# Kernel optimization log

Measured on AMD Instinct MI355X. Metric: run time of the kernel, lower is better.

## Reference

```python
import jax, jax.numpy as jnp
import numpy as np

EMBED_DIM = 256
NUM_HEADS = 8
HEAD_DIM = 32
BIAS_HIDDEN = 64
LN_EPS = 1e-5


def setup_inputs() -> dict:
    key = jax.random.key(0)
    ks = jax.random.split(key, 12)
    B, N = 2, 1024
    inner = NUM_HEADS * HEAD_DIM  # 256
    inp = {
        'x': jax.random.normal(ks[0], (B, N, EMBED_DIM), dtype=jnp.float32),
        'coords': jax.random.normal(ks[1], (B, N, 2), dtype=jnp.float32),
        'velocities': jax.random.normal(ks[2], (B, N, 2), dtype=jnp.float32),
        # LayerNorm params
        'ln_g': jnp.ones((EMBED_DIM,), jnp.float32),
        'ln_b': jnp.zeros((EMBED_DIM,), jnp.float32),
        # qkv projection (no bias)
        'w_qkv': jax.random.normal(ks[3], (EMBED_DIM, 3 * inner), dtype=jnp.float32) * (EMBED_DIM ** -0.5),
        # output projection
        'w_o': jax.random.normal(ks[4], (inner, EMBED_DIM), dtype=jnp.float32) * (inner ** -0.5),
        'b_o': jnp.zeros((EMBED_DIM,), jnp.float32),
        # relational bias MLP: Linear(5,64) -> GELU -> Linear(64, num_heads)
        'w1': jax.random.normal(ks[5], (5, BIAS_HIDDEN), dtype=jnp.float32) * (5 ** -0.5),
        'b1': jnp.zeros((BIAS_HIDDEN,), jnp.float32),
        'w2': jax.random.normal(ks[6], (BIAS_HIDDEN, NUM_HEADS), dtype=jnp.float32) * (BIAS_HIDDEN ** -0.5),
        'b2': jnp.zeros((NUM_HEADS,), jnp.float32),
    }
    return inp


def _rope_sin_cos(n, dim):
    half = dim // 2  # rotary applied over half pairs
    inv_freq = 1.0 / (10000.0 ** (jnp.arange(0, half, dtype=jnp.float32) / half))
    freqs = jnp.arange(n, dtype=jnp.float32)[:, None] * inv_freq[None, :]  # [n, half]
    return jnp.sin(freqs), jnp.cos(freqs)


def _apply_rope(t, sin, cos):
    d = t.shape[-1]
    t1, t2 = t[..., : d // 2], t[..., d // 2 :]
    return jnp.concatenate([t1 * cos - t2 * sin, t2 * cos + t1 * sin], axis=-1)


def reference(x, coords, velocities, ln_g, ln_b, w_qkv, w_o, b_o, w1, b1, w2, b2):
    b, n, _ = x.shape
    # LayerNorm
    mu = jnp.mean(x, axis=-1, keepdims=True)
    var = jnp.mean((x - mu) ** 2, axis=-1, keepdims=True)
    h = (x - mu) / jnp.sqrt(var + LN_EPS) * ln_g + ln_b
    # qkv
    qkv = h @ w_qkv  # [b, n, 3*inner]
    inner = NUM_HEADS * HEAD_DIM
    q, k, v = jnp.split(qkv, 3, axis=-1)
    reshape_heads = lambda t: t.reshape(b, n, NUM_HEADS, HEAD_DIM).transpose(0, 2, 1, 3)
    q, k, v = reshape_heads(q), reshape_heads(k), reshape_heads(v)  # [b,h,n,d]
    sin, cos = _rope_sin_cos(n, HEAD_DIM)  # [n, d//2], broadcast over b,h
    q = _apply_rope(q, sin, cos)
    k = _apply_rope(k, sin, cos)
    scale = HEAD_DIM ** -0.5
    scores = jnp.einsum('bhnd,bhmd->bhnm', q, k) * scale  # [b,h,n,n] fp32
    # relational bias: pairwise MLP over [dx(2), |dx|(1), dv(2)]
    dx = coords[:, :, None, :] - coords[:, None, :, :]        # [b,n,n,2]
    dist = jnp.linalg.norm(dx, axis=-1, keepdims=True)        # [b,n,n,1]
    dv = velocities[:, :, None, :] - velocities[:, None, :, :]
    feats = jnp.concatenate([dx, dist, dv], axis=-1)          # [b,n,n,5]
    hid = jax.nn.gelu(feats @ w1 + b1, approximate=False)     # [b,n,n,64]
    rel = (hid @ w2 + b2).transpose(0, 3, 1, 2)               # [b,h,n,n]
    scores = scores + rel
    probs = jax.nn.softmax(scores, axis=-1)
    probs = jnp.nan_to_num(probs, nan=0.0)
    out = jnp.einsum('bhnm,bhmd->bhnd', probs, v)
    out = out.transpose(0, 2, 1, 3).reshape(b, n, inner)
    return out @ w_o + b_o
```

## Files before the change

kernel.cpp:

```cpp
#include <hip/hip_runtime.h>
#include <hip/hip_bf16.h>
#include <hip/hip_fp16.h>
#include <math.h>
#include <string.h>

typedef _Float16 half8 __attribute__((ext_vector_type(8)));
typedef _Float16 half4 __attribute__((ext_vector_type(4)));
typedef float floatx4 __attribute__((ext_vector_type(4)));
typedef float floatx16 __attribute__((ext_vector_type(16)));

#if defined(__has_builtin) && __has_builtin(__builtin_amdgcn_mfma_f32_16x16x16f16)
#define MFMA_PV(a, b, c) __builtin_amdgcn_mfma_f32_16x16x16f16((a), (b), (c), 0, 0, 0)
#else
__device__ __forceinline__ floatx4 mfma_pv_asm(half4 a, half4 b, floatx4 c) {
  floatx4 d;
  asm volatile("v_mfma_f32_16x16x16_f16 %0, %1, %2, %3"
               : "=v"(d) : "v"(a), "v"(b), "v"(c));
  return d;
}
#define MFMA_PV(a, b, c) mfma_pv_asm((a), (b), (c))
#endif

__device__ __forceinline__ floatx16 MFMA_S1(half4 a, half4 b, floatx16 c) {
#if defined(__has_builtin) && __has_builtin(__builtin_amdgcn_mfma_f32_32x32x8f16)
  return __builtin_amdgcn_mfma_f32_32x32x8f16(a, b, c, 0, 0, 0);
#else
  floatx16 d;
  asm volatile("v_mfma_f32_32x32x8_f16 %0, %1, %2, %3"
               : "=v"(d) : "v"(a), "v"(b), "v"(c));
  return d;
#endif
}

__device__ __forceinline__ floatx16 MFMA_S2(half8 a, half8 b, floatx16 c) {
#if defined(__has_builtin) && __has_builtin(__builtin_amdgcn_mfma_f32_32x32x16_f16)
  return __builtin_amdgcn_mfma_f32_32x32x16_f16(a, b, c, 0, 0, 0);
#else
  floatx16 d;
  asm volatile("v_mfma_f32_32x32x16_f16 %0, %1, %2, %3"
               : "=v"(d) : "v"(a), "v"(b), "v"(c));
  return d;
#endif
}

__device__ __forceinline__ float gelu_exact(float z) {
  return 0.5f * z * (1.0f + erff(z * 0.70710678118654752f));
}
__device__ __forceinline__ unsigned int packh2(float a, float b) {
  __half2 h = __halves2half2(__float2half_rn(a), __float2half_rn(b));
  unsigned int u;
  memcpy(&u, &h, 4);
  return u;
}

__global__ __launch_bounds__(256) void prep_kernel(
    const float* __restrict__ x, const float* __restrict__ g,
    const float* __restrict__ bv, __half* __restrict__ h16,
    const float* __restrict__ w_qkv, const float* __restrict__ w_o,
    const float* __restrict__ w1, const float* __restrict__ b1,
    const float* __restrict__ w2,
    __half* __restrict__ wqT, __half* __restrict__ woT,
    unsigned int* __restrict__ gtabu, uint2* __restrict__ A1g,
    uint4* __restrict__ A2g) {
  int t = threadIdx.x;
  if (blockIdx.x < 2048) {
    int row = blockIdx.x;
    float v = x[(size_t)row * 256 + t];
    float s = v, q = v * v;
#pragma unroll
    for (int o = 32; o > 0; o >>= 1) {
      s += __shfl_xor(s, o);
      q += __shfl_xor(q, o);
    }
    __shared__ float ss[4], qq[4];
    int w = t >> 6, l = t & 63;
    if (l == 0) { ss[w] = s; qq[w] = q; }
    __syncthreads();
    s = ss[0] + ss[1] + ss[2] + ss[3];
    q = qq[0] + qq[1] + qq[2] + qq[3];
    float mu = s * (1.f / 256.f);
    float var = q * (1.f / 256.f) - mu * mu;
    float inv = rsqrtf(var + 1e-5f);
    h16[(size_t)row * 256 + t] = __float2half_rn((v - mu) * inv * g[t] + bv[t]);
    return;
  }
  int bx = blockIdx.x - 2048;
  if (bx < 768) {
    wqT[(size_t)bx * 256 + t] = __float2half_rn(w_qkv[(size_t)t * 768 + bx]);
  } else if (bx < 1024) {
    int n = bx - 768;
    woT[(size_t)n * 256 + t] = __float2half_rn(w_o[(size_t)t * 256 + n]);
  } else if (bx == 1024) {
#pragma unroll
    for (int s = 0; s < 8; s++) {
      int e = t * 8 + s;
      float z = -16.f + (float)e * (1.f / 64.f);
      float g0 = gelu_exact(z);
      float g1 = gelu_exact(z + (1.f / 64.f));
      gtabu[e] = packh2(g0, g1 - g0);
    }
  } else {
    if (t < 128) {
      int hb = t >> 6, l = t & 63;
      int hid = hb * 32 + (l & 31);
      float v[4];
#pragma unroll
      for (int e = 0; e < 4; e++) {
        int k = (l >> 5) * 4 + e;
        v[e] = (k < 5) ? w1[k * 64 + hid] : ((k == 5) ? b1[hid] : 0.f);
      }
      A1g[t] = make_uint2(packh2(v[0], v[1]), packh2(v[2], v[3]));
    }
    {
      int c = t >> 6, l = t & 63;
      int row = l & 31;
      int lh = l >> 5;
      float v[8];
#pragma unroll
      for (int e = 0; e < 8; e++) {
        int hid = c * 16 + (e & 3) + 8 * (e >> 2) + 4 * lh;
        v[e] = (row < 8) ? w2[hid * 8 + row] : 0.f;
      }
      A2g[t] = make_uint4(packh2(v[0], v[1]), packh2(v[2], v[3]),
                          packh2(v[4], v[5]), packh2(v[6], v[7]));
    }
  }
}

__global__ __launch_bounds__(256) void qkv_rope(
    const __half* __restrict__ h16, const __half* __restrict__ wqT,
    __half* __restrict__ qo, __half* __restrict__ ko, __half* __restrict__ vo) {
  int wave = blockIdx.x * 4 + (threadIdx.x >> 6);
  int mt = wave / 24, nt = wave - mt * 24;
  int l = threadIdx.x & 63;
  int c31 = l & 31, kg = l >> 5;
  int m0 = mt * 32, n0 = nt * 32;
  floatx16 acc0 = {0.f}, acc1 = {0.f};
  const _Float16* ap = (const _Float16*)h16 + (size_t)(m0 + c31) * 256 + kg * 8;
  const _Float16* bp = (const _Float16*)wqT + (size_t)(n0 + c31) * 256 + kg * 8;
  for (int k0 = 0; k0 < 256; k0 += 32) {
    half8 a0 = *(const half8*)(ap + k0);
    half8 b0 = *(const half8*)(bp + k0);
    half8 a1 = *(const half8*)(ap + k0 + 16);
    half8 b1 = *(const half8*)(bp + k0 + 16);
    acc0 = MFMA_S2(a0, b0, acc0);
    acc1 = MFMA_S2(a1, b1, acc1);
  }
  floatx16 acc = acc0 + acc1;

  if (nt < 16) {
    __half* dst = (nt < 8) ? qo : ko;
    float qscale = (nt < 8) ? 0.17677669529663687f : 1.0f;
    int hh = nt & 7;
    int f = c31 & 15;
    float inv_freq = exp2f((float)f * -0.8304820237218407f);
#pragma unroll
    for (int r = 0; r < 16; r++) {
      float part = __shfl_xor(acc[r], 16);
      int m = m0 + (r & 3) + 8 * (r >> 2) + 4 * kg;
      int nseq = m & 1023, bb = m >> 10;
      float sn, cs;
      __sincosf((float)nseq * inv_freq, &sn, &cs);
      float out = (c31 < 16) ? (acc[r] * cs - part * sn)
                             : (acc[r] * cs + part * sn);
      dst[((size_t)(bb * 8 + hh) * 1024 + nseq) * 32 + c31] =
          __float2half_rn(out * qscale);
    }
  } else {
    int hh = nt - 16;
#pragma unroll
    for (int r = 0; r < 16; r++) {
      int m = m0 + (r & 3) + 8 * (r >> 2) + 4 * kg;
      int nseq = m & 1023, bb = m >> 10;
      vo[((size_t)(bb * 8 + hh) * 1024 + nseq) * 32 + c31] = __float2half_rn(acc[r]);
    }
  }
}

__device__ __forceinline__ _Float16 gelu_tab16(float z, const unsigned int* gt) {
  float tf = __builtin_amdgcn_fmed3f(fmaf(z, 64.f, 1024.f), 0.f, 2047.f);
  float fr = __builtin_amdgcn_fractf(tf);
  unsigned int e = gt[(unsigned int)tf];
  union { unsigned int u; _Float16 h[2]; } cv;
  cv.u = e;
  return (_Float16)(cv.h[0] + (_Float16)fr * cv.h[1]);
}

__global__ __launch_bounds__(512) void fused_attn(
    const __half* __restrict__ qh, const __half* __restrict__ kh,
    const __half* __restrict__ vh,
    const float* __restrict__ coords, const float* __restrict__ vels,
    const unsigned int* __restrict__ gtabu, const uint2* __restrict__ A1g,
    const uint4* __restrict__ A2g, const float* __restrict__ b2,
    float* __restrict__ Opart, float* __restrict__ ml) {
  __shared__ unsigned int gtab[2048];
  __shared__ __half relS[8][64][18];
  const int t = threadIdx.x;
  for (int e = t; e < 2048; e += 512) gtab[e] = gtabu[e];

  const int js = blockIdx.x & 7;
  const int it = (blockIdx.x >> 3) & 63;
  const int b  = blockIdx.x >> 9;
  const int h  = t >> 6;
  const int lane = t & 63;
  const int lg = lane >> 4, li16 = lane & 15;
  const int li = lane & 31, lh = lane >> 5;
  const int i0 = it * 16;
  const size_t bh = (size_t)(b * 8 + h) * 1024;

  float b2v0 = b2[4 * lh + 0], b2v1 = b2[4 * lh + 1];
  float b2v2 = b2[4 * lh + 2], b2v3 = b2[4 * lh + 3];

  const half8 qf = *(const half8*)((const _Float16*)qh + (bh + i0 + li16) * 32 + 8 * lg);
  floatx4 accLo = {0.f, 0.f, 0.f, 0.f};
  floatx4 accHi = {0.f, 0.f, 0.f, 0.f};
  float m_run = -3.0e38f, l_run = 0.f;

  __syncthreads();

  for (int chunk = 0; chunk < 2; chunk++) {
    const int jt = js * 128 + chunk * 64;
    {
      uint2 a1u0 = A1g[lane], a1u1 = A1g[64 + lane];
      uint4 a2u0 = A2g[lane], a2u1 = A2g[64 + lane];
      uint4 a2u2 = A2g[128 + lane], a2u3 = A2g[192 + lane];
#pragma unroll
      for (int tt = 0; tt < 4; tt++) {
        const int i_loc = 2 * h + (tt >> 1);
        const int jsub = tt & 1;
        const int i = i0 + i_loc;
        const int j = jt + jsub * 32 + li;
        float2 ci = *(const float2*)&coords[(size_t)(b * 1024 + i) * 2];
        float2 vi = *(const float2*)&vels[(size_t)(b * 1024 + i) * 2];
        float2 cj = *(const float2*)&coords[(size_t)(b * 1024 + j) * 2];
        float2 vj = *(const float2*)&vels[(size_t)(b * 1024 + j) * 2];
        float dx0 = ci.x - cj.x, dx1 = ci.y - cj.y;
        float dv0 = vi.x - vj.x, dv1 = vi.y - vj.y;
        float dist = sqrtf(dx0 * dx0 + dx1 * dx1);
        half4 bf;
        bf[0] = lh ? (_Float16)dv1 : (_Float16)dx0;
        bf[1] = lh ? (_Float16)1.0f : (_Float16)dx1;
        bf[2] = lh ? (_Float16)0.0f : (_Float16)dist;
        bf[3] = lh ? (_Float16)0.0f : (_Float16)dv0;

        floatx16 zinit = {0.f};
        floatx16 acc = {0.f};
        {
          floatx16 z0 = MFMA_S1(*(half4*)&a1u0, bf, zinit);
          unsigned int u[8] __attribute__((aligned(16)));
#pragma unroll
          for (int q = 0; q < 8; q++) {
            _Float16 ga = gelu_tab16(z0[2 * q], gtab);
            _Float16 gb = gelu_tab16(z0[2 * q + 1], gtab);
            union { unsigned int uu; _Float16 hx[2]; } cv;
            cv.hx[0] = ga; cv.hx[1] = gb;
            u[q] = cv.uu;
          }
          acc = MFMA_S2(*(half8*)&a2u0, *(half8*)&u[0], acc);
          acc = MFMA_S2(*(half8*)&a2u1, *(half8*)&u[4], acc);
        }
        {
          floatx16 z1 = MFMA_S1(*(half4*)&a1u1, bf, zinit);
          unsigned int u[8] __attribute__((aligned(16)));
#pragma unroll
          for (int q = 0; q < 8; q++) {
            _Float16 ga = gelu_tab16(z1[2 * q], gtab);
            _Float16 gb = gelu_tab16(z1[2 * q + 1], gtab);
            union { unsigned int uu; _Float16 hx[2]; } cv;
            cv.hx[0] = ga; cv.hx[1] = gb;
            u[q] = cv.uu;
          }
          acc = MFMA_S2(*(half8*)&a2u2, *(half8*)&u[0], acc);
          acc = MFMA_S2(*(half8*)&a2u3, *(half8*)&u[4], acc);
        }
        const int jc = jsub * 32 + li;
        relS[4 * lh + 0][jc][i_loc] = __float2half_rn(acc[0] + b2v0);
        relS[4 * lh + 1][jc][i_loc] = __float2half_rn(acc[1] + b2v1);
        relS[4 * lh + 2][jc][i_loc] = __float2half_rn(acc[2] + b2v2);
        relS[4 * lh + 3][jc][i_loc] = __float2half_rn(acc[3] + b2v3);
      }
    }
    __syncthreads();
    {
      const _Float16* kb = (const _Float16*)kh + (bh + jt + li16) * 32 + 8 * lg;
      half8 kf0 = *(const half8*)(kb + 0 * 512);
      half8 kf1 = *(const half8*)(kb + 1 * 512);
      half8 kf2 = *(const half8*)(kb + 2 * 512);
      half8 kf3 = *(const half8*)(kb + 3 * 512);
      floatx4 c0, c1, c2, c3;
#pragma unroll
      for (int r = 0; r < 4; r++) {
        c0[r] = __half2float(relS[h][0 + 4 * lg + r][li16]);
        c1[r] = __half2float(relS[h][16 + 4 * lg + r][li16]);
        c2[r] = __half2float(relS[h][32 + 4 * lg + r][li16]);
        c3[r] = __half2float(relS[h][48 + 4 * lg + r][li16]);
      }
      __builtin_amdgcn_s_setprio(1);
      floatx4 st0 = __builtin_amdgcn_mfma_f32_16x16x32_f16(kf0, qf, c0, 0, 0, 0);
      floatx4 st1 = __builtin_amdgcn_mfma_f32_16x16x32_f16(kf1, qf, c1, 0, 0, 0);
      floatx4 st2 = __builtin_amdgcn_mfma_f32_16x16x32_f16(kf2, qf, c2, 0, 0, 0);
      floatx4 st3 = __builtin_amdgcn_mfma_f32_16x16x32_f16(kf3, qf, c3, 0, 0, 0);
      __builtin_amdgcn_s_setprio(0);
      float s[16];
#pragma unroll
      for (int r = 0; r < 4; r++) {
        s[0 + r] = st0[r]; s[4 + r] = st1[r];
        s[8 + r] = st2[r]; s[12 + r] = st3[r];
      }
      float tm = fmaxf(fmaxf(fmaxf(s[0], s[1]), fmaxf(s[2], s[3])),
                       fmaxf(fmaxf(s[4], s[5]), fmaxf(s[6], s[7])));
      tm = fmaxf(tm, fmaxf(fmaxf(fmaxf(s[8], s[9]), fmaxf(s[10], s[11])),
                           fmaxf(fmaxf(s[12], s[13]), fmaxf(s[14], s[15]))));
      tm = fmaxf(tm, __shfl_xor(tm, 16));
      tm = fmaxf(tm, __shfl_xor(tm, 32));
      float nm = fmaxf(m_run, tm);
      float fc = __expf(m_run - nm);
      float p[16];
#pragma unroll
      for (int e = 0; e < 16; e++) p[e] = __expf(s[e] - nm);
      float ts = ((p[0] + p[1]) + (p[2] + p[3])) + ((p[4] + p[5]) + (p[6] + p[7]));
      ts += ((p[8] + p[9]) + (p[10] + p[11])) + ((p[12] + p[13]) + (p[14] + p[15]));
      ts += __shfl_xor(ts, 16);
      ts += __shfl_xor(ts, 32);
      l_run = l_run * fc + ts;
      m_run = nm;
      float fT0 = __shfl(fc, 4 * lg + 0);
      float fT1 = __shfl(fc, 4 * lg + 1);
      float fT2 = __shfl(fc, 4 * lg + 2);
      float fT3 = __shfl(fc, 4 * lg + 3);
      accLo[0] *= fT0; accHi[0] *= fT0;
      accLo[1] *= fT1; accHi[1] *= fT1;
      accLo[2] *= fT2; accHi[2] *= fT2;
      accLo[3] *= fT3; accHi[3] *= fT3;
#pragma unroll
      for (int tt = 0; tt < 4; tt++) {
        half4 pf;
        pf[0] = (_Float16)p[4 * tt + 0];
        pf[1] = (_Float16)p[4 * tt + 1];
        pf[2] = (_Float16)p[4 * tt + 2];
        pf[3] = (_Float16)p[4 * tt + 3];
        const _Float16* vb = (const _Float16*)vh + (bh + jt + tt * 16 + 4 * lg) * 32 + li16;
        half4 vf0, vf1;
        vf0[0] = vb[0];  vf0[1] = vb[32]; vf0[2] = vb[64]; vf0[3] = vb[96];
        vf1[0] = vb[16]; vf1[1] = vb[48]; vf1[2] = vb[80]; vf1[3] = vb[112];
        __builtin_amdgcn_s_setprio(1);
        accLo = MFMA_PV(pf, vf0, accLo);
        accHi = MFMA_PV(pf, vf1, accHi);
        __builtin_amdgcn_s_setprio(0);
      }
    }
    __syncthreads();
  }
  size_t orow = (size_t)(b * 8 + js) * 1024 + i0 + 4 * lg;
#pragma unroll
  for (int r = 0; r < 4; r++) {
    float* op = Opart + (orow + r) * 256 + h * 32 + li16;
    op[0] = accLo[r];
    op[16] = accHi[r];
  }
  if (lane < 16) {
    ((float2*)ml)[((size_t)(b * 8 + js) * 1024 + i0 + lane) * 8 + h] =
        make_float2(m_run, l_run);
  }
}

__global__ __launch_bounds__(256) void combine_proj(
    const float* __restrict__ Opart, const float* __restrict__ ml,
    const __half* __restrict__ woT, const float* __restrict__ b_o,
    float* __restrict__ out) {
  __shared__ _Float16 As[16][264];
  const int r0 = blockIdx.x * 8;
  const int t = threadIdx.x;
  const int hh = t >> 5;
#pragma unroll
  for (int rr = 8; rr < 16; rr++) As[rr][t] = (_Float16)0.f;
#pragma unroll
  for (int rr = 0; rr < 8; rr++) {
    int row = r0 + rr;
    int b = row >> 10, i = row & 1023;
    float2 mls[8];
    float M = -1e30f;
#pragma unroll
    for (int js = 0; js < 8; js++) {
      mls[js] = ((const float2*)ml)[(((size_t)(b * 8 + js) * 1024) + i) * 8 + hh];
      M = fmaxf(M, mls[js].x);
    }
    float L = 0.f, Ov = 0.f;
#pragma unroll
    for (int js = 0; js < 8; js++) {
      float w = __expf(mls[js].x - M);
      L += mls[js].y * w;
      Ov += Opart[(((size_t)(b * 8 + js) * 1024) + i) * 256 + t] * w;
    }
    As[rr][t] = (_Float16)(Ov / L);
  }
  __syncthreads();
  const int wv = t >> 6, lane = t & 63;
  const int lg = lane >> 4, li = lane & 15;
#pragma unroll
  for (int nt = 0; nt < 4; nt++) {
    int n0 = (wv * 4 + nt) * 16;
    floatx4 acc = {0.f, 0.f, 0.f, 0.f};
    const _Float16* bp = (const _Float16*)woT + (size_t)(n0 + li) * 256 + 8 * lg;
#pragma unroll
    for (int k0 = 0; k0 < 256; k0 += 32) {
      half8 af = *(const half8*)&As[li][k0 + 8 * lg];
      half8 bf = *(const half8*)(bp + k0);
      acc = __builtin_amdgcn_mfma_f32_16x16x32_f16(af, bf, acc, 0, 0, 0);
    }
    float bb = b_o[n0 + li];
#pragma unroll
    for (int r = 0; r < 4; r++) {
      int mrow = 4 * lg + r;
      if (mrow < 8) out[(size_t)(r0 + mrow) * 256 + n0 + li] = acc[r] + bb;
    }
  }
}

extern "C" void kernel_launch(void* const* d_in, const int* in_sizes, int n_in,
                              void* d_out, int out_size, void* d_ws, size_t ws_size,
                              hipStream_t stream) {
  const float* x      = (const float*)d_in[0];
  const float* coords = (const float*)d_in[1];
  const float* vels   = (const float*)d_in[2];
  const float* ln_g   = (const float*)d_in[3];
  const float* ln_b   = (const float*)d_in[4];
  const float* w_qkv  = (const float*)d_in[5];
  const float* w_o    = (const float*)d_in[6];
  const float* b_o    = (const float*)d_in[7];
  const float* w1     = (const float*)d_in[8];
  const float* b1     = (const float*)d_in[9];
  const float* w2     = (const float*)d_in[10];
  const float* b2     = (const float*)d_in[11];
  float* out = (float*)d_out;

  char* wsb = (char*)d_ws;
  float* Opart = (float*)wsb;
  __half* wqT  = (__half*)(wsb + 16777216);
  __half* woT  = (__half*)(wsb + 17170432);
  unsigned int* gtab = (unsigned int*)(wsb + 17301504);
  uint2* A1g   = (uint2*)(wsb + 17317888);
  uint4* A2g   = (uint4*)(wsb + 17318912);
  __half* h16  = (__half*)(wsb + 17825792);
  __half* qh   = (__half*)(wsb + 18874368);
  __half* kh   = (__half*)(wsb + 19922944);
  __half* vh   = (__half*)(wsb + 20971520);
  float* ml    = (float*)(wsb + 22020096);

  prep_kernel<<<3074, 256, 0, stream>>>(x, ln_g, ln_b, h16, w_qkv, w_o,
                                        w1, b1, w2, wqT, woT, gtab, A1g, A2g);
  qkv_rope<<<384, 256, 0, stream>>>(h16, wqT, qh, kh, vh);
  fused_attn<<<1024, 512, 0, stream>>>(qh, kh, vh, coords, vels, gtab,
                                       A1g, A2g, b2, Opart, ml);
  combine_proj<<<256, 256, 0, stream>>>(Opart, ml, woT, b_o, out);
}
```

Before: 79.99 us.

## Double-buffer relational bias tile and overlap MLP with attention phase

Doubles the shared bias buffer so the bias MLP for the second key chunk is computed while the first chunk's QK/softmax/PV phase runs. This removes one of the block barriers and lets MFMA and gather work from the two phases interleave. The bias-MLP weight fragments are also loaded once before the chunks instead of once per chunk. In exchange, shared memory use and register pressure go up, which may lower occupancy.

```diff
diff --git a/kernel.cpp b/kernel.cpp
--- a/kernel.cpp
+++ b/kernel.cpp
@@ -194,7 +194,7 @@
     const uint4* __restrict__ A2g, const float* __restrict__ b2,
     float* __restrict__ Opart, float* __restrict__ ml) {
   __shared__ unsigned int gtab[2048];
-  __shared__ __half relS[8][64][18];
+  __shared__ __half relS[2][8][64][18];
   const int t = threadIdx.x;
   for (int e = t; e < 2048; e += 512) gtab[e] = gtabu[e];
 
@@ -216,141 +216,150 @@
   floatx4 accHi = {0.f, 0.f, 0.f, 0.f};
   float m_run = -3.0e38f, l_run = 0.f;
 
+  uint2 a1u0 = A1g[lane], a1u1 = A1g[64 + lane];
+  uint4 a2u0 = A2g[lane], a2u1 = A2g[64 + lane];
+  uint4 a2u2 = A2g[128 + lane], a2u3 = A2g[192 + lane];
+
+#define PHASE_A(CHUNK, BUF)                                                    \
+  {                                                                            \
+    const int jtA = js * 128 + (CHUNK) * 64;                                   \
+    _Pragma("unroll")                                                          \
+    for (int tt = 0; tt < 4; tt++) {                                           \
+      const int i_loc = 2 * h + (tt >> 1);                                     \
+      const int jsub = tt & 1;                                                 \
+      const int iA = i0 + i_loc;                                               \
+      const int jA = jtA + jsub * 32 + li;                                     \
+      float2 ci = *(const float2*)&coords[(size_t)(b * 1024 + iA) * 2];        \
+      float2 vi = *(const float2*)&vels[(size_t)(b * 1024 + iA) * 2];          \
+      float2 cj = *(const float2*)&coords[(size_t)(b * 1024 + jA) * 2];        \
+      float2 vj = *(const float2*)&vels[(size_t)(b * 1024 + jA) * 2];          \
+      float dx0 = ci.x - cj.x, dx1 = ci.y - cj.y;                              \
+      float dv0 = vi.x - vj.x, dv1 = vi.y - vj.y;                              \
+      float dist = sqrtf(dx0 * dx0 + dx1 * dx1);                               \
+      half4 bf;                                                                \
+      bf[0] = lh ? (_Float16)dv1 : (_Float16)dx0;                              \
+      bf[1] = lh ? (_Float16)1.0f : (_Float16)dx1;                             \
+      bf[2] = lh ? (_Float16)0.0f : (_Float16)dist;                            \
+      bf[3] = lh ? (_Float16)0.0f : (_Float16)dv0;                             \
+      floatx16 zinit = {0.f};                                                  \
+      floatx16 acc = {0.f};                                                    \
+      {                                                                        \
+        floatx16 z0 = MFMA_S1(*(half4*)&a1u0, bf, zinit);                      \
+        unsigned int u[8] __attribute__((aligned(16)));                        \
+        _Pragma("unroll")                                                      \
+        for (int q = 0; q < 8; q++) {                                          \
+          _Float16 ga = gelu_tab16(z0[2 * q], gtab);                           \
+          _Float16 gb = gelu_tab16(z0[2 * q + 1], gtab);                       \
+          union { unsigned int uu; _Float16 hx[2]; } cv;                       \
+          cv.hx[0] = ga; cv.hx[1] = gb;                                        \
+          u[q] = cv.uu;                                                        \
+        }                                                                      \
+        acc = MFMA_S2(*(half8*)&a2u0, *(half8*)&u[0], acc);                    \
+        acc = MFMA_S2(*(half8*)&a2u1, *(half8*)&u[4], acc);                    \
+      }                                                                        \
+      {                                                                        \
+        floatx16 z1 = MFMA_S1(*(half4*)&a1u1, bf, zinit);                      \
+        unsigned int u[8] __attribute__((aligned(16)));                        \
+        _Pragma("unroll")                                                      \
+        for (int q = 0; q < 8; q++) {                                          \
+          _Float16 ga = gelu_tab16(z1[2 * q], gtab);                           \
+          _Float16 gb = gelu_tab16(z1[2 * q + 1], gtab);                       \
+          union { unsigned int uu; _Float16 hx[2]; } cv;                       \
+          cv.hx[0] = ga; cv.hx[1] = gb;                                        \
+          u[q] = cv.uu;                                                        \
+        }                                                                      \
+        acc = MFMA_S2(*(half8*)&a2u2, *(half8*)&u[0], acc);                    \
+        acc = MFMA_S2(*(half8*)&a2u3, *(half8*)&u[4], acc);                    \
+      }                                                                        \
+      const int jc = jsub * 32 + li;                                           \
+      relS[BUF][4 * lh + 0][jc][i_loc] = __float2half_rn(acc[0] + b2v0);       \
+      relS[BUF][4 * lh + 1][jc][i_loc] = __float2half_rn(acc[1] + b2v1);       \
+      relS[BUF][4 * lh + 2][jc][i_loc] = __float2half_rn(acc[2] + b2v2);       \
+      relS[BUF][4 * lh + 3][jc][i_loc] = __float2half_rn(acc[3] + b2v3);       \
+    }                                                                          \
+  }
+
+#define PHASE_B(CHUNK, BUF)                                                    \
+  {                                                                            \
+    const int jtB = js * 128 + (CHUNK) * 64;                                   \
+    const _Float16* kb = (const _Float16*)kh + (bh + jtB + li16) * 32 + 8 * lg;\
+    half8 kf0 = *(const half8*)(kb + 0 * 512);                                 \
+    half8 kf1 = *(const half8*)(kb + 1 * 512);                                 \
+    half8 kf2 = *(const half8*)(kb + 2 * 512);                                 \
+    half8 kf3 = *(const half8*)(kb + 3 * 512);                                 \
+    floatx4 c0, c1, c2, c3;                                                    \
+    _Pragma("unroll")                                                          \
+    for (int r = 0; r < 4; r++) {                                              \
+      c0[r] = __half2float(relS[BUF][h][0 + 4 * lg + r][li16]);                \
+      c1[r] = __half2float(relS[BUF][h][16 + 4 * lg + r][li16]);               \
+      c2[r] = __half2float(relS[BUF][h][32 + 4 * lg + r][li16]);               \
+      c3[r] = __half2float(relS[BUF][h][48 + 4 * lg + r][li16]);               \
+    }                                                                          \
+    __builtin_amdgcn_s_setprio(1);                                             \
+    floatx4 st0 = __builtin_amdgcn_mfma_f32_16x16x32_f16(kf0, qf, c0, 0, 0, 0);\
+    floatx4 st1 = __builtin_amdgcn_mfma_f32_16x16x32_f16(kf1, qf, c1, 0, 0, 0);\
+    floatx4 st2 = __builtin_amdgcn_mfma_f32_16x16x32_f16(kf2, qf, c2, 0, 0, 0);\
+    floatx4 st3 = __builtin_amdgcn_mfma_f32_16x16x32_f16(kf3, qf, c3, 0, 0, 0);\
+    __builtin_amdgcn_s_setprio(0);                                             \
+    float s[16];                                                               \
+    _Pragma("unroll")                                                          \
+    for (int r = 0; r < 4; r++) {                                              \
+      s[0 + r] = st0[r]; s[4 + r] = st1[r];                                    \
+      s[8 + r] = st2[r]; s[12 + r] = st3[r];                                   \
+    }                                                                          \
+    float tm = fmaxf(fmaxf(fmaxf(s[0], s[1]), fmaxf(s[2], s[3])),              \
+                     fmaxf(fmaxf(s[4], s[5]), fmaxf(s[6], s[7])));             \
+    tm = fmaxf(tm, fmaxf(fmaxf(fmaxf(s[8], s[9]), fmaxf(s[10], s[11])),        \
+                         fmaxf(fmaxf(s[12], s[13]), fmaxf(s[14], s[15]))));    \
+    tm = fmaxf(tm, __shfl_xor(tm, 16));                                        \
+    tm = fmaxf(tm, __shfl_xor(tm, 32));                                        \
+    float nm = fmaxf(m_run, tm);                                               \
+    float fc = __expf(m_run - nm);                                             \
+    float p[16];                                                               \
+    _Pragma("unroll")                                                          \
+    for (int e = 0; e < 16; e++) p[e] = __expf(s[e] - nm);                     \
+    float ts = ((p[0] + p[1]) + (p[2] + p[3])) + ((p[4] + p[5]) + (p[6] + p[7]));\
+    ts += ((p[8] + p[9]) + (p[10] + p[11])) + ((p[12] + p[13]) + (p[14] + p[15]));\
+    ts += __shfl_xor(ts, 16);                                                  \
+    ts += __shfl_xor(ts, 32);                                                  \
+    l_run = l_run * fc + ts;                                                   \
+    m_run = nm;                                                                \
+    float fT0 = __shfl(fc, 4 * lg + 0);                                        \
+    float fT1 = __shfl(fc, 4 * lg + 1);                                        \
+    float fT2 = __shfl(fc, 4 * lg + 2);                                        \
+    float fT3 = __shfl(fc, 4 * lg + 3);                                        \
+    accLo[0] *= fT0; accHi[0] *= fT0;                                          \
+    accLo[1] *= fT1; accHi[1] *= fT1;                                          \
+    accLo[2] *= fT2; accHi[2] *= fT2;                                          \
+    accLo[3] *= fT3; accHi[3] *= fT3;                                          \
+    _Pragma("unroll")                                                          \
+    for (int tt = 0; tt < 4; tt++) {                                           \
+      half4 pf;                                                                \
+      pf[0] = (_Float16)p[4 * tt + 0];                                         \
+      pf[1] = (_Float16)p[4 * tt + 1];                                         \
+      pf[2] = (_Float16)p[4 * tt + 2];                                         \
+      pf[3] = (_Float16)p[4 * tt + 3];                                         \
+      const _Float16* vb = (const _Float16*)vh + (bh + jtB + tt * 16 + 4 * lg) * 32 + li16;\
+      half4 vf0, vf1;                                                          \
+      vf0[0] = vb[0];  vf0[1] = vb[32]; vf0[2] = vb[64]; vf0[3] = vb[96];      \
+      vf1[0] = vb[16]; vf1[1] = vb[48]; vf1[2] = vb[80]; vf1[3] = vb[112];     \
+      __builtin_amdgcn_s_setprio(1);                                           \
+      accLo = MFMA_PV(pf, vf0, accLo);                                         \
+      accHi = MFMA_PV(pf, vf1, accHi);                                         \
+      __builtin_amdgcn_s_setprio(0);                                           \
+    }                                                                          \
+  }
+
   __syncthreads();
-
-  for (int chunk = 0; chunk < 2; chunk++) {
-    const int jt = js * 128 + chunk * 64;
-    {
-      uint2 a1u0 = A1g[lane], a1u1 = A1g[64 + lane];
-      uint4 a2u0 = A2g[lane], a2u1 = A2g[64 + lane];
-      uint4 a2u2 = A2g[128 + lane], a2u3 = A2g[192 + lane];
-#pragma unroll
-      for (int tt = 0; tt < 4; tt++) {
-        const int i_loc = 2 * h + (tt >> 1);
-        const int jsub = tt & 1;
-        const int i = i0 + i_loc;
-        const int j = jt + jsub * 32 + li;
-        float2 ci = *(const float2*)&coords[(size_t)(b * 1024 + i) * 2];
-        float2 vi = *(const float2*)&vels[(size_t)(b * 1024 + i) * 2];
-        float2 cj = *(const float2*)&coords[(size_t)(b * 1024 + j) * 2];
-        float2 vj = *(const float2*)&vels[(size_t)(b * 1024 + j) * 2];
-        float dx0 = ci.x - cj.x, dx1 = ci.y - cj.y;
-        float dv0 = vi.x - vj.x, dv1 = vi.y - vj.y;
-        float dist = sqrtf(dx0 * dx0 + dx1 * dx1);
-        half4 bf;
-        bf[0] = lh ? (_Float16)dv1 : (_Float16)dx0;
-        bf[1] = lh ? (_Float16)1.0f : (_Float16)dx1;
-        bf[2] = lh ? (_Float16)0.0f : (_Float16)dist;
-        bf[3] = lh ? (_Float16)0.0f : (_Float16)dv0;
-
-        floatx16 zinit = {0.f};
-        floatx16 acc = {0.f};
-        {
-          floatx16 z0 = MFMA_S1(*(half4*)&a1u0, bf, zinit);
-          unsigned int u[8] __attribute__((aligned(16)));
-#pragma unroll
-          for (int q = 0; q < 8; q++) {
-            _Float16 ga = gelu_tab16(z0[2 * q], gtab);
-            _Float16 gb = gelu_tab16(z0[2 * q + 1], gtab);
-            union { unsigned int uu; _Float16 hx[2]; } cv;
-            cv.hx[0] = ga; cv.hx[1] = gb;
-            u[q] = cv.uu;
-          }
-          acc = MFMA_S2(*(half8*)&a2u0, *(half8*)&u[0], acc);
-          acc = MFMA_S2(*(half8*)&a2u1, *(half8*)&u[4], acc);
-        }
-        {
-          floatx16 z1 = MFMA_S1(*(half4*)&a1u1, bf, zinit);
-          unsigned int u[8] __attribute__((aligned(16)));
-#pragma unroll
-          for (int q = 0; q < 8; q++) {
-            _Float16 ga = gelu_tab16(z1[2 * q], gtab);
-            _Float16 gb = gelu_tab16(z1[2 * q + 1], gtab);
-            union { unsigned int uu; _Float16 hx[2]; } cv;
-            cv.hx[0] = ga; cv.hx[1] = gb;
-            u[q] = cv.uu;
-          }
-          acc = MFMA_S2(*(half8*)&a2u2, *(half8*)&u[0], acc);
-          acc = MFMA_S2(*(half8*)&a2u3, *(half8*)&u[4], acc);
-        }
-        const int jc = jsub * 32 + li;
-        relS[4 * lh + 0][jc][i_loc] = __float2half_rn(acc[0] + b2v0);
-        relS[4 * lh + 1][jc][i_loc] = __float2half_rn(acc[1] + b2v1);
-        relS[4 * lh + 2][jc][i_loc] = __float2half_rn(acc[2] + b2v2);
-        relS[4 * lh + 3][jc][i_loc] = __float2half_rn(acc[3] + b2v3);
-      }
-    }
-    __syncthreads();
-    {
-      const _Float16* kb = (const _Float16*)kh + (bh + jt + li16) * 32 + 8 * lg;
-      half8 kf0 = *(const half8*)(kb + 0 * 512);
-      half8 kf1 = *(const half8*)(kb + 1 * 512);
-      half8 kf2 = *(const half8*)(kb + 2 * 512);
-      half8 kf3 = *(const half8*)(kb + 3 * 512);
-      floatx4 c0, c1, c2, c3;
-#pragma unroll
-      for (int r = 0; r < 4; r++) {
-        c0[r] = __half2float(relS[h][0 + 4 * lg + r][li16]);
-        c1[r] = __half2float(relS[h][16 + 4 * lg + r][li16]);
-        c2[r] = __half2float(relS[h][32 + 4 * lg + r][li16]);
-        c3[r] = __half2float(relS[h][48 + 4 * lg + r][li16]);
-      }
-      __builtin_amdgcn_s_setprio(1);
-      floatx4 st0 = __builtin_amdgcn_mfma_f32_16x16x32_f16(kf0, qf, c0, 0, 0, 0);
-      floatx4 st1 = __builtin_amdgcn_mfma_f32_16x16x32_f16(kf1, qf, c1, 0, 0, 0);
-      floatx4 st2 = __builtin_amdgcn_mfma_f32_16x16x32_f16(kf2, qf, c2, 0, 0, 0);
-      floatx4 st3 = __builtin_amdgcn_mfma_f32_16x16x32_f16(kf3, qf, c3, 0, 0, 0);
-      __builtin_amdgcn_s_setprio(0);
-      float s[16];
-#pragma unroll
-      for (int r = 0; r < 4; r++) {
-        s[0 + r] = st0[r]; s[4 + r] = st1[r];
-        s[8 + r] = st2[r]; s[12 + r] = st3[r];
-      }
-      float tm = fmaxf(fmaxf(fmaxf(s[0], s[1]), fmaxf(s[2], s[3])),
-                       fmaxf(fmaxf(s[4], s[5]), fmaxf(s[6], s[7])));
-      tm = fmaxf(tm, fmaxf(fmaxf(fmaxf(s[8], s[9]), fmaxf(s[10], s[11])),
-                           fmaxf(fmaxf(s[12], s[13]), fmaxf(s[14], s[15]))));
-      tm = fmaxf(tm, __shfl_xor(tm, 16));
-      tm = fmaxf(tm, __shfl_xor(tm, 32));
-      float nm = fmaxf(m_run, tm);
-      float fc = __expf(m_run - nm);
-      float p[16];
-#pragma unroll
-      for (int e = 0; e < 16; e++) p[e] = __expf(s[e] - nm);
-      float ts = ((p[0] + p[1]) + (p[2] + p[3])) + ((p[4] + p[5]) + (p[6] + p[7]));
-      ts += ((p[8] + p[9]) + (p[10] + p[11])) + ((p[12] + p[13]) + (p[14] + p[15]));
-      ts += __shfl_xor(ts, 16);
-      ts += __shfl_xor(ts, 32);
-      l_run = l_run * fc + ts;
-      m_run = nm;
-      float fT0 = __shfl(fc, 4 * lg + 0);
-      float fT1 = __shfl(fc, 4 * lg + 1);
-      float fT2 = __shfl(fc, 4 * lg + 2);
-      float fT3 = __shfl(fc, 4 * lg + 3);
-      accLo[0] *= fT0; accHi[0] *= fT0;
-      accLo[1] *= fT1; accHi[1] *= fT1;
-      accLo[2] *= fT2; accHi[2] *= fT2;
-      accLo[3] *= fT3; accHi[3] *= fT3;
-#pragma unroll
-      for (int tt = 0; tt < 4; tt++) {
-        half4 pf;
-        pf[0] = (_Float16)p[4 * tt + 0];
-        pf[1] = (_Float16)p[4 * tt + 1];
-        pf[2] = (_Float16)p[4 * tt + 2];
-        pf[3] = (_Float16)p[4 * tt + 3];
-        const _Float16* vb = (const _Float16*)vh + (bh + jt + tt * 16 + 4 * lg) * 32 + li16;
-        half4 vf0, vf1;
-        vf0[0] = vb[0];  vf0[1] = vb[32]; vf0[2] = vb[64]; vf0[3] = vb[96];
-        vf1[0] = vb[16]; vf1[1] = vb[48]; vf1[2] = vb[80]; vf1[3] = vb[112];
-        __builtin_amdgcn_s_setprio(1);
-        accLo = MFMA_PV(pf, vf0, accLo);
-        accHi = MFMA_PV(pf, vf1, accHi);
-        __builtin_amdgcn_s_setprio(0);
-      }
-    }
-    __syncthreads();
-  }
+  PHASE_A(0, 0)
+  __syncthreads();
+  PHASE_A(1, 1)
+  PHASE_B(0, 0)
+  __syncthreads();
+  PHASE_B(1, 1)
+#undef PHASE_A
+#undef PHASE_B
+
   size_t orow = (size_t)(b * 8 + js) * 1024 + i0 + 4 * lg;
 #pragma unroll
   for (int r = 0; r < 4; r++) {
```

New measurement: 81.14 us. No clear change (+1.4%).
